# Kernel tuning notes

Measured on AMD Instinct MI355X. Metric: run time of the kernel, lower is better.

Reference implementation:

```python
import jax, jax.numpy as jnp
import numpy as np

N = 20000        # atoms in batch
E = 640000       # edges (avg degree 32)
NG = 1000        # molecules (graphs)
H = 128          # hidden_channels = num_filters
G = 50           # num_gaussians
L = 6            # num_interactions
CUTOFF = 10.0
LOG2 = float(np.log(2.0))


def ssp(x):
    # ShiftedSoftplus: softplus(x) - log(2)
    return jax.nn.softplus(x) - jnp.asarray(LOG2, x.dtype)


def setup_inputs() -> dict:
    key = jax.random.key(0)
    ks = jax.random.split(key, 16)
    pos = jax.random.normal(ks[0], (N, 3), dtype=jnp.float32) * 3.0
    z = jax.random.randint(ks[1], (N,), 1, 100)  # avoid padding_idx 0
    batch = jnp.sort(jax.random.randint(ks[2], (N,), 0, NG))
    edge_index = jax.random.randint(ks[3], (2, E), 0, N)
    # avoid self-loops (zero distance -> nan grad of norm)
    row, col = edge_index[0], edge_index[1]
    col = jnp.where(col == row, (col + 1) % N, col)
    edge_index = jnp.stack([row, col])

    def lin(k, fi, fo, stacked=False):
        shape = (L, fi, fo) if stacked else (fi, fo)
        return (jax.random.normal(k, shape, dtype=jnp.float32) / np.sqrt(fi)).astype(jnp.float32)

    emb = jax.random.normal(ks[4], (100, H), dtype=jnp.float32)
    emb = emb.at[0].set(0.0)  # padding_idx=0
    inp = {
        "pos": pos, "z": z, "batch": batch, "edge_index": edge_index,
        "emb": emb,
        "mlp_w1": lin(ks[5], G, H, True), "mlp_b1": jnp.zeros((L, H), jnp.float32),
        "mlp_w2": lin(ks[6], H, H, True), "mlp_b2": jnp.zeros((L, H), jnp.float32),
        "aw_w": lin(ks[7], H, H, True), "aw_b": jnp.zeros((L, H), jnp.float32),
        "out_w1": lin(ks[8], H, H, True), "out_b1": jnp.zeros((L, H), jnp.float32),
        "out_w2": lin(ks[9], H, H, True), "out_b2": jnp.zeros((L, H), jnp.float32),
        "head_w1": lin(ks[10], H, H // 2), "head_b1": jnp.zeros((H // 2,), jnp.float32),
        "head_w2": lin(ks[11], H // 2, 1), "head_b2": jnp.zeros((1,), jnp.float32),
    }
    return inp


def reference(pos, z, batch, edge_index, emb,
              mlp_w1, mlp_b1, mlp_w2, mlp_b2,
              aw_w, aw_b, out_w1, out_b1, out_w2, out_b2,
              head_w1, head_b1, head_w2, head_b2):
    row, col = edge_index[0], edge_index[1]
    # edge distances
    diff = pos[row] - pos[col]                       # [E,3]
    d = jnp.sqrt(jnp.sum(diff * diff, axis=-1))      # [E]
    # Gaussian smearing
    offset = jnp.linspace(0.0, CUTOFF, G)
    coeff = -0.5 / (offset[1] - offset[0]) ** 2
    ea = jnp.exp(coeff * (d[:, None] - offset[None, :]) ** 2)  # [E,G]
    # cosine cutoff
    C = 0.5 * (jnp.cos(d * jnp.pi / CUTOFF) + 1.0)             # [E]

    h = emb[z]                                                 # [N,H]
    for l in range(L):
        hw = h @ aw_w[l] + aw_b[l]                             # atom-wise linear
        W = ssp(ssp(ea @ mlp_w1[l] + mlp_b1[l]) @ mlp_w2[l] + mlp_b2[l]) * C[:, None]  # [E,H]
        msg = hw[row] * W                                      # gather + filter
        conv = jax.ops.segment_sum(msg, col, num_segments=N)   # scatter-add to targets
        upd = ssp(conv @ out_w1[l] + out_b1[l]) @ out_w2[l] + out_b2[l]
        h = h + upd                                            # residual
    y = ssp(h @ head_w1 + head_b1) @ head_w2 + head_b2         # [N,1]
    return jax.ops.segment_sum(y, batch, num_segments=NG)      # [NG,1]
```

## Files before the change

### kernel.cpp

```cpp
#include <hip/hip_runtime.h>
#include <math.h>

#define HID 128
#define NG_GAUSS 50
#define TBL_P 8192
#define TBL_DMAX 12.8f
#define TBL_DT (TBL_DMAX / (float)TBL_P)
#define TBL_INV_DT ((float)TBL_P / TBL_DMAX)
#define PI_F 3.14159265358979323846f
#define NB 8

typedef short bf16x8 __attribute__((ext_vector_type(8)));
typedef float f32x4 __attribute__((ext_vector_type(4)));

__device__ __forceinline__ float ssp_f(float x) {
  float e = __expf(-fabsf(x));
  return fmaxf(x, 0.f) + __logf(1.f + e) - 0.69314718055994530942f;
}
__device__ __forceinline__ unsigned short f2bf(float x) {
  unsigned u = __float_as_uint(x);
  unsigned r = (u + 0x7FFFu + ((u >> 16) & 1u)) >> 16;
  return (unsigned short)r;
}

__global__ __launch_bounds__(256) void k_edge_pre(
    const float* __restrict__ pos, const int* __restrict__ ei,
    int E, int* __restrict__ epack, int* __restrict__ deg)
{
  int e = blockIdx.x * 256 + threadIdx.x;
  if (e >= E) return;
  int r = ei[e];
  int c = ei[E + e];
  float dx = pos[3*r+0] - pos[3*c+0];
  float dy = pos[3*r+1] - pos[3*c+1];
  float dz = pos[3*r+2] - pos[3*c+2];
  float d = sqrtf(dx*dx + dy*dy + dz*dz);
  int i0 = (int)(d * TBL_INV_DT + 0.5f);
  if (i0 >= TBL_P) { epack[e] = -1; return; }
  epack[e] = (r << 13) | i0;
  atomicAdd(&deg[c * NB + (r >> 12)], 1);
}

__global__ __launch_bounds__(1024) void k_scan1(
    const int* __restrict__ deg, int* __restrict__ ptr,
    int* __restrict__ bsum, int M)
{
  __shared__ int wsum[16];
  int base = blockIdx.x * 2048;
  int t = threadIdx.x;
  int i0 = base + 2 * t;
  int v0 = (i0 < M) ? deg[i0] : 0;
  int v1 = (i0 + 1 < M) ? deg[i0 + 1] : 0;
  int s = v0 + v1;
  int lane = t & 63, w = t >> 6;
  int ps = s;
  for (int o = 1; o < 64; o <<= 1) { int x = __shfl_up(ps, o); if (lane >= o) ps += x; }
  if (lane == 63) wsum[w] = ps;
  __syncthreads();
  if (w == 0 && lane < 16) {
    int v = wsum[lane];
    int pv = v;
    for (int o = 1; o < 16; o <<= 1) { int x = __shfl_up(pv, o); if (lane >= o) pv += x; }
    wsum[lane] = pv - v;
  }
  __syncthreads();
  int ex = wsum[w] + ps - s;
  if (i0 < M) ptr[i0] = ex;
  if (i0 + 1 < M) ptr[i0 + 1] = ex + v0;
  if (t == 1023) bsum[blockIdx.x] = ex + s;
}

__global__ __launch_bounds__(1024) void k_scan2(int* __restrict__ bsum, int G)
{
  __shared__ int wsum[16];
  int t = threadIdx.x;
  int s = (t < G) ? bsum[t] : 0;
  int lane = t & 63, w = t >> 6;
  int ps = s;
  for (int o = 1; o < 64; o <<= 1) { int x = __shfl_up(ps, o); if (lane >= o) ps += x; }
  if (lane == 63) wsum[w] = ps;
  __syncthreads();
  if (w == 0 && lane < 16) {
    int v = wsum[lane];
    int pv = v;
    for (int o = 1; o < 16; o <<= 1) { int x = __shfl_up(pv, o); if (lane >= o) pv += x; }
    wsum[lane] = pv - v;
  }
  __syncthreads();
  int ex = wsum[w] + ps - s;
  if (t < G) bsum[t] = ex;
  if (t == G - 1) bsum[G] = ex + s;
}

__global__ __launch_bounds__(1024) void k_scan3(
    int* __restrict__ ptr, const int* __restrict__ bsum, int M, int G)
{
  int base = blockIdx.x * 2048;
  int t = threadIdx.x;
  int add = bsum[blockIdx.x];
  int i0 = base + 2 * t;
  if (i0 < M) ptr[i0] += add;
  if (i0 + 1 < M) ptr[i0 + 1] += add;
  if (blockIdx.x == 0 && t == 0) ptr[M] = bsum[G];
}

__global__ __launch_bounds__(256) void k_csr_scatter(
    const int* __restrict__ col, const int* __restrict__ epack,
    const int* __restrict__ ptr, int* __restrict__ cursor,
    int* __restrict__ csr, int E)
{
  int e = blockIdx.x * 256 + threadIdx.x;
  if (e >= E) return;
  int p = epack[e];
  if (p < 0) return;
  int c = col[e];
  int idx = c * NB + ((p >> 13) >> 12);
  int slot = ptr[idx] + atomicAdd(&cursor[idx], 1);
  csr[slot] = p;
}

__global__ __launch_bounds__(256) void k_wprep(
    const float* __restrict__ aw_w, const float* __restrict__ out_w1,
    const float* __restrict__ out_w2, const float* __restrict__ mlp_w2,
    const float* __restrict__ mlp_w1, const float* __restrict__ head_w1,
    unsigned short* __restrict__ awt, unsigned short* __restrict__ o1t,
    unsigned short* __restrict__ o2t, unsigned short* __restrict__ m2t,
    unsigned short* __restrict__ m1t, unsigned short* __restrict__ hwt)
{
  __shared__ float Wl[64][132];
  int l = blockIdx.x, t = blockIdx.y;
  int k0 = blockIdx.z * 64;
  const float* src; unsigned short* dst; int K; int NCOL = 128;
  switch (t) {
    case 0:  src = aw_w;   dst = awt; K = 128; break;
    case 1:  src = out_w1; dst = o1t; K = 128; break;
    case 2:  src = out_w2; dst = o2t; K = 128; break;
    case 3:  src = mlp_w2; dst = m2t; K = 128; break;
    case 4:  src = mlp_w1; dst = m1t; K = NG_GAUSS; break;
    default:
      if (l) return;
      src = head_w1; dst = hwt; K = 128; NCOL = 64; break;
  }
  src += (long)l * K * NCOL;
  dst += (long)l * 128 * 128;
  const int tid = threadIdx.x;
  for (int idx = tid; idx < 64 * 128; idx += 256) {
    int kk = idx >> 7, n = idx & 127;
    int k = k0 + kk;
    Wl[kk][n] = (k < K && n < NCOL) ? src[(long)k * NCOL + n] : 0.f;
  }
  __syncthreads();
  for (int idx = tid; idx < 128 * 8; idx += 256) {
    int n = idx >> 3, pl = idx & 7;
    int p = (k0 >> 3) + pl;
    int q = p ^ (n & 7);
    int kk = (q << 3) - k0;
    ushort4 lo = make_ushort4(f2bf(Wl[kk+0][n]), f2bf(Wl[kk+1][n]),
                              f2bf(Wl[kk+2][n]), f2bf(Wl[kk+3][n]));
    ushort4 hi = make_ushort4(f2bf(Wl[kk+4][n]), f2bf(Wl[kk+5][n]),
                              f2bf(Wl[kk+6][n]), f2bf(Wl[kk+7][n]));
    *(ushort4*)(dst + ((long)n << 7) + (p << 3)) = lo;
    *(ushort4*)(dst + ((long)n << 7) + (p << 3) + 4) = hi;
  }
}

__global__ void k_ea_build(unsigned short* __restrict__ EA)
{
  int p = blockIdx.x;
  int g = threadIdx.x;
  float v = 0.f;
  if (g < NG_GAUSS) {
    float step = 10.0f / 49.0f;
    float off = g * step;
    float coeff = -0.5f / (step * step);
    float t = p * TBL_DT - off;
    v = __expf(coeff * t * t);
  }
  EA[p * 128 + g] = f2bf(v);
}

__global__ __launch_bounds__(256) void k_h_init(
    const float4* __restrict__ emb4, const int* __restrict__ z,
    float4* __restrict__ h4, ushort4* __restrict__ hb4, int N)
{
  int idx = blockIdx.x * 256 + threadIdx.x;
  if (idx >= N * 32) return;
  int n = idx >> 5, c = idx & 31;
  float4 v = emb4[z[n] * 32 + c];
  h4[idx] = v;
  hb4[idx] = make_ushort4(f2bf(v.x), f2bf(v.y), f2bf(v.z), f2bf(v.w));
}

__global__ __launch_bounds__(256) void k_fused(
    const unsigned short* __restrict__ X, long xstr,
    const unsigned short* __restrict__ Wa, long wastr,
    const float* __restrict__ ba, long bastr,
    const unsigned short* __restrict__ Wb, long wbstr,
    const float* __restrict__ bb, long bbstr,
    const float* __restrict__ R,
    void* __restrict__ out1, long o1str, int o1_bf16, int actB, int mulC,
    float dscale,
    const unsigned short* __restrict__ Wc, const float* __restrict__ bc,
    unsigned short* __restrict__ out2,
    const float* __restrict__ hw2, const float* __restrict__ hb2,
    const int* __restrict__ batchp, float* __restrict__ outp,
    int M)
{
  __shared__ unsigned short Xs[32][128];
  __shared__ unsigned short Wbuf[128][128];

  const int l = blockIdx.y;
  const int m0 = blockIdx.x * 32;
  const int tid = threadIdx.x;
  const unsigned short* Xb = X + (long)l * xstr;

  for (int idx = tid; idx < 512; idx += 256) {
    int r = idx >> 4, c = idx & 15;
    int m = m0 + r;
    int4 v = make_int4(0, 0, 0, 0);
    if (m < M) v = *(const int4*)(Xb + (long)m * 128 + c * 8);
    *(int4*)&Xs[r][(c ^ (r & 7)) << 3] = v;
  }
  {
    const unsigned short* W0 = Wa ? (Wa + (long)l * wastr) : (Wb + (long)l * wbstr);
    const int4* s = (const int4*)W0;
    int4* d = (int4*)Wbuf;
    for (int i = tid; i < 2048; i += 256) d[i] = s[i];
  }
  __syncthreads();

  const int wv = tid >> 6, lane = tid & 63;
  const int wr = wv >> 1, wc = wv & 1;
  const int lr = lane & 15, lk = lane >> 4;
  const int arow = (wr << 4) | lr;

  f32x4 acc[4];
  auto zacc = [&]() {
#pragma unroll
    for (int i = 0; i < 4; ++i)
#pragma unroll
      for (int j = 0; j < 4; ++j) acc[i][j] = 0.f;
  };
  auto gemm = [&]() {
#pragma unroll
    for (int kc = 0; kc < 4; ++kc) {
      int q = (kc << 2) | lk;
      bf16x8 a = *(const bf16x8*)&Xs[arow][(q ^ (arow & 7)) << 3];
#pragma unroll
      for (int nt = 0; nt < 4; ++nt) {
        int n = (wc << 6) | (nt << 4) | lr;
        bf16x8 b = *(const bf16x8*)(&Wbuf[0][0] + n * 128 + ((q ^ (n & 7)) << 3));
        acc[nt] = __builtin_amdgcn_mfma_f32_16x16x32_bf16(a, b, acc[nt], 0, 0, 0);
      }
    }
  };

  if (Wa) {
    const float* bab = ba + (long)l * bastr;
    zacc();
    gemm();
    __syncthreads();
#pragma unroll
    for (int nt = 0; nt < 4; ++nt) {
      int col = (wc << 6) | (nt << 4) | lr;
      float bv = bab[col];
#pragma unroll
      for (int r2 = 0; r2 < 4; ++r2) {
        int row = (wr << 4) | (lk << 2) | r2;
        float v2 = ssp_f(acc[nt][r2] + bv);
        int cch = col >> 3;
        Xs[row][((cch ^ (row & 7)) << 3) | (col & 7)] = f2bf(v2);
      }
    }
    {
      const int4* s = (const int4*)(Wb + (long)l * wbstr);
      int4* d = (int4*)Wbuf;
      for (int i = tid; i < 2048; i += 256) d[i] = s[i];
    }
    __syncthreads();
  }

  const float* bbb = bb + (long)l * bbstr;
  zacc();
  gemm();
  __syncthreads();

#pragma unroll
  for (int nt = 0; nt < 4; ++nt) {
    int col = (wc << 6) | (nt << 4) | lr;
    float bv = bbb[col];
#pragma unroll
    for (int r2 = 0; r2 < 4; ++r2) {
      int row = (wr << 4) | (lk << 2) | r2;
      int m = m0 + row;
      float v2 = acc[nt][r2] + bv;
      if (actB) v2 = ssp_f(v2);
      if (R && m < M) v2 += R[(long)m * 128 + col];
      if (mulC) {
        float d = (float)m * dscale;
        v2 *= 0.5f * (__cosf(d * (PI_F / 10.0f)) + 1.0f);
      }
      if (m < M && out1) {
        if (o1_bf16)
          ((unsigned short*)out1)[(long)l * o1str + (long)m * 128 + col] = f2bf(v2);
        else
          ((float*)out1)[(long)l * o1str + (long)m * 128 + col] = v2;
      }
      if (Wc) {
        int cch = col >> 3;
        Xs[row][((cch ^ (row & 7)) << 3) | (col & 7)] = f2bf(v2);
      }
    }
  }

  if (Wc) {
    {
      const int4* s = (const int4*)Wc;
      int4* d = (int4*)Wbuf;
      for (int i = tid; i < 2048; i += 256) d[i] = s[i];
    }
    __syncthreads();
    zacc();
    gemm();
    if (hw2) {
      if (wc == 0) {
        float b1v[4], w2v[4];
#pragma unroll
        for (int nt = 0; nt < 4; ++nt) {
          int col = (nt << 4) | lr;
          b1v[nt] = bc[col];
          w2v[nt] = hw2[col];
        }
        float bias2 = hb2[0];
#pragma unroll
        for (int r2 = 0; r2 < 4; ++r2) {
          float sv = 0.f;
#pragma unroll
          for (int nt = 0; nt < 4; ++nt)
            sv += ssp_f(acc[nt][r2] + b1v[nt]) * w2v[nt];
          sv += __shfl_xor(sv, 1);
          sv += __shfl_xor(sv, 2);
          sv += __shfl_xor(sv, 4);
          sv += __shfl_xor(sv, 8);
          if (lr == 0) {
            int m = m0 + (wr << 4) + (lk << 2) + r2;
            if (m < M) atomicAdd(&outp[batchp[m]], sv + bias2);
          }
        }
      }
    } else {
#pragma unroll
      for (int nt = 0; nt < 4; ++nt) {
        int col = (wc << 6) | (nt << 4) | lr;
        float bv = bc[col];
#pragma unroll
        for (int r2 = 0; r2 < 4; ++r2) {
          int row = (wr << 4) | (lk << 2) | r2;
          int m = m0 + row;
          if (m < M)
            out2[(long)m * 128 + col] = f2bf(acc[nt][r2] + bv);
        }
      }
    }
  }
}

__global__ __launch_bounds__(256) void k_conv(
    const int* __restrict__ csr, const int* __restrict__ ptr,
    const unsigned short* __restrict__ T, const unsigned short* __restrict__ hw,
    unsigned short* __restrict__ convb, int N)
{
  int wid = __builtin_amdgcn_readfirstlane((blockIdx.x * 256 + threadIdx.x) >> 6);
  int lane = threadIdx.x & 63;
  if (wid >= N) return;
  int s = __builtin_amdgcn_readfirstlane(ptr[wid * NB]);
  int e = __builtin_amdgcn_readfirstlane(ptr[wid * NB + NB]);
  const int la = lane << 1;
  float ax[8], ay[8];
#pragma unroll
  for (int i = 0; i < 8; ++i) { ax[i] = 0.f; ay[i] = 0.f; }
  int j = s;
  if (j + 8 <= e) {
    int cc[8];
#pragma unroll
    for (int i = 0; i < 8; ++i) cc[i] = __builtin_amdgcn_readfirstlane(csr[j + i]);
    for (; j + 16 <= e; j += 8) {
      unsigned tv[8], hv[8];
#pragma unroll
      for (int i = 0; i < 8; ++i) {
        unsigned pr = (unsigned)cc[i];
        tv[i] = *(const unsigned*)(T + ((size_t)(pr & 8191u) << 7) + la);
        hv[i] = *(const unsigned*)(hw + ((size_t)(pr >> 13) << 7) + la);
      }
#pragma unroll
      for (int i = 0; i < 8; ++i) cc[i] = __builtin_amdgcn_readfirstlane(csr[j + 8 + i]);
#pragma unroll
      for (int i = 0; i < 8; ++i) {
        float w0 = __uint_as_float(tv[i] << 16), w1 = __uint_as_float(tv[i] & 0xffff0000u);
        float h0 = __uint_as_float(hv[i] << 16), h1 = __uint_as_float(hv[i] & 0xffff0000u);
        ax[i] = fmaf(w0, h0, ax[i]); ay[i] = fmaf(w1, h1, ay[i]);
      }
    }
    {
      unsigned tv[8], hv[8];
#pragma unroll
      for (int i = 0; i < 8; ++i) {
        unsigned pr = (unsigned)cc[i];
        tv[i] = *(const unsigned*)(T + ((size_t)(pr & 8191u) << 7) + la);
        hv[i] = *(const unsigned*)(hw + ((size_t)(pr >> 13) << 7) + la);
      }
#pragma unroll
      for (int i = 0; i < 8; ++i) {
        float w0 = __uint_as_float(tv[i] << 16), w1 = __uint_as_float(tv[i] & 0xffff0000u);
        float h0 = __uint_as_float(hv[i] << 16), h1 = __uint_as_float(hv[i] & 0xffff0000u);
        ax[i] = fmaf(w0, h0, ax[i]); ay[i] = fmaf(w1, h1, ay[i]);
      }
    }
    j += 8;
  }
  for (; j < e; ++j) {
    unsigned pr = (unsigned)__builtin_amdgcn_readfirstlane(csr[j]);
    unsigned tv = *(const unsigned*)(T + ((size_t)(pr & 8191u) << 7) + la);
    unsigned hv = *(const unsigned*)(hw + ((size_t)(pr >> 13) << 7) + la);
    float w0 = __uint_as_float(tv << 16), w1 = __uint_as_float(tv & 0xffff0000u);
    float h0 = __uint_as_float(hv << 16), h1 = __uint_as_float(hv & 0xffff0000u);
    ax[0] = fmaf(w0, h0, ax[0]); ay[0] = fmaf(w1, h1, ay[0]);
  }
  float axs = ((ax[0] + ax[1]) + (ax[2] + ax[3])) + ((ax[4] + ax[5]) + (ax[6] + ax[7]));
  float ays = ((ay[0] + ay[1]) + (ay[2] + ay[3])) + ((ay[4] + ay[5]) + (ay[6] + ay[7]));
  unsigned outw = (unsigned)f2bf(axs) | ((unsigned)f2bf(ays) << 16);
  *(unsigned*)(convb + ((size_t)wid << 7) + la) = outw;
}

extern "C" void kernel_launch(void* const* d_in, const int* in_sizes, int n_in,
                              void* d_out, int out_size, void* d_ws, size_t ws_size,
                              hipStream_t stream) {
  (void)n_in; (void)ws_size;
  const float* pos     = (const float*)d_in[0];
  const int*   z       = (const int*)d_in[1];
  const int*   batch   = (const int*)d_in[2];
  const int*   ei      = (const int*)d_in[3];
  const float* emb     = (const float*)d_in[4];
  const float* mlp_w1  = (const float*)d_in[5];
  const float* mlp_b1  = (const float*)d_in[6];
  const float* mlp_w2  = (const float*)d_in[7];
  const float* mlp_b2  = (const float*)d_in[8];
  const float* aw_w    = (const float*)d_in[9];
  const float* aw_b    = (const float*)d_in[10];
  const float* out_w1  = (const float*)d_in[11];
  const float* out_b1  = (const float*)d_in[12];
  const float* out_w2  = (const float*)d_in[13];
  const float* out_b2  = (const float*)d_in[14];
  const float* head_w1 = (const float*)d_in[15];
  const float* head_b1 = (const float*)d_in[16];
  const float* head_w2 = (const float*)d_in[17];
  const float* head_b2 = (const float*)d_in[18];

  const int N  = in_sizes[0] / 3;
  const int E  = in_sizes[3] / 2;
  const int NG = out_size;
  const int L  = in_sizes[5] / (NG_GAUSS * HID);

  char* ws = (char*)d_ws;
  size_t off = 0;
  auto alloc = [&](size_t bytes) -> void* {
    off = (off + 255) & ~(size_t)255;
    void* p = ws + off;
    off += bytes;
    return p;
  };

  const size_t nh = (size_t)N * HID;
  float* h_buf = (float*)alloc(nh * 4 > (size_t)E * 4 ? nh * 4 : (size_t)E * 4);
  int*   epack = (int*)h_buf;
  unsigned short* hb    = (unsigned short*)alloc(nh * 2);
  unsigned short* hw    = (unsigned short*)alloc(nh * 2);
  unsigned short* convb = (unsigned short*)alloc(
      nh * 2 > (size_t)TBL_P * 128 * 2 ? nh * 2 : (size_t)TBL_P * 128 * 2);
  unsigned short* EA    = convb;
  int* csr = (int*)alloc((size_t)E * 4);
  unsigned short* T   = (unsigned short*)alloc((size_t)L * TBL_P * 128 * 2);
  unsigned short* awt = (unsigned short*)alloc((size_t)L * 16384 * 2);
  unsigned short* o1t = (unsigned short*)alloc((size_t)L * 16384 * 2);
  unsigned short* o2t = (unsigned short*)alloc((size_t)L * 16384 * 2);
  unsigned short* m2t = (unsigned short*)alloc((size_t)L * 16384 * 2);
  unsigned short* m1t = (unsigned short*)alloc((size_t)L * 16384 * 2);
  unsigned short* hwt = (unsigned short*)alloc((size_t)16384 * 2);
  int* deg    = (int*)alloc((size_t)N * NB * 4);
  int* ptr    = (int*)alloc(((size_t)N * NB + 1) * 4);
  int* cursor = (int*)alloc((size_t)N * NB * 4);
  int* bsum   = (int*)alloc((size_t)1024 * 4);

  const int M = N * NB;
  const int G = (M + 2047) / 2048;

  hipMemsetAsync(deg, 0, (size_t)M * 4, stream);
  hipMemsetAsync(cursor, 0, (size_t)M * 4, stream);
  hipMemsetAsync(d_out, 0, (size_t)NG * 4, stream);

  int egrid = (E + 255) / 256;
  k_edge_pre<<<egrid, 256, 0, stream>>>(pos, ei, E, epack, deg);
  k_scan1<<<G, 1024, 0, stream>>>(deg, ptr, bsum, M);
  k_scan2<<<1, 1024, 0, stream>>>(bsum, G);
  k_scan3<<<G, 1024, 0, stream>>>(ptr, bsum, M, G);
  k_csr_scatter<<<egrid, 256, 0, stream>>>(ei + E, epack, ptr, cursor, csr, E);

  k_wprep<<<dim3(L, 6, 2), 256, 0, stream>>>(aw_w, out_w1, out_w2, mlp_w2,
                                             mlp_w1, head_w1,
                                             awt, o1t, o2t, m2t, m1t, hwt);
  k_ea_build<<<TBL_P, 128, 0, stream>>>(EA);

  k_fused<<<dim3(TBL_P / 32, L), 256, 0, stream>>>(
      EA, 0L,
      m1t, 16384L, mlp_b1, 128L,
      m2t, 16384L, mlp_b2, 128L,
      (const float*)0,
      T, (long)TBL_P * 128, 1 , 1 , 1 , TBL_DT,
      (const unsigned short*)0, (const float*)0, (unsigned short*)0,
      (const float*)0, (const float*)0, (const int*)0, (float*)0,
      TBL_P);

  k_h_init<<<(N * 32 + 255) / 256, 256, 0, stream>>>(
      (const float4*)emb, z, (float4*)h_buf, (ushort4*)hb, N);

  const int ngrid = (N + 31) / 32;
  const int wgrid = (N * 64 + 255) / 256;

  k_fused<<<dim3(ngrid, 1), 256, 0, stream>>>(
      hb, 0L,
      (const unsigned short*)0, 0L, (const float*)0, 0L,
      awt, 0L, aw_b, 0L,
      (const float*)0,
      hw, 0L, 1 , 0, 0, 0.f,
      (const unsigned short*)0, (const float*)0, (unsigned short*)0,
      (const float*)0, (const float*)0, (const int*)0, (float*)0,
      N);

  for (int l = 0; l < L; ++l) {
    k_conv<<<wgrid, 256, 0, stream>>>(
        csr, ptr, T + (size_t)l * TBL_P * 128, hw, convb, N);
    const int last = (l + 1 == L);
    const unsigned short* Wc = last ? hwt : (awt + (size_t)(l + 1) * 16384);
    const float* bc = last ? head_b1 : (aw_b + (size_t)(l + 1) * 128);
    k_fused<<<dim3(ngrid, 1), 256, 0, stream>>>(
        convb, 0L,
        o1t + (size_t)l * 16384, 0L, out_b1 + (size_t)l * 128, 0L,
        o2t + (size_t)l * 16384, 0L, out_b2 + (size_t)l * 128, 0L,
        h_buf,
        last ? (void*)0 : (void*)h_buf, 0L, 0 , 0 , 0, 0.f,
        Wc, bc, last ? (unsigned short*)0 : hw,
        last ? head_w2 : (const float*)0, last ? head_b2 : (const float*)0,
        last ? batch : (const int*)0, last ? (float*)d_out : (float*)0,
        N);
  }
}
```

Before: 389.5 us.

## Store residual state in bf16, halve filter table, and refine CSR source buckets

The residual hidden state h is now kept only in bf16 and updated in place in the fused update kernel. This replaces the fp32 h buffer plus its separate bf16 copy and cuts residual read/write traffic. The distance lookup table shrinks from 8192 to 4096 points, so the per-layer filter table gathered in the conv kernel is smaller and more cache-resident, at the cost of coarser distance resolution. The CSR source bucketing doubles from 8 to 16 buckets per target to improve gather locality on hw. Accumulating the residual in bf16 across six layers risks a loss of accuracy.

```diff
diff --git a/kernel.cpp b/kernel.cpp
--- a/kernel.cpp
+++ b/kernel.cpp
@@ -3,12 +3,13 @@
 
 #define HID 128
 #define NG_GAUSS 50
-#define TBL_P 8192
+#define TBL_P 4096
 #define TBL_DMAX 12.8f
 #define TBL_DT (TBL_DMAX / (float)TBL_P)
 #define TBL_INV_DT ((float)TBL_P / TBL_DMAX)
 #define PI_F 3.14159265358979323846f
-#define NB 8
+#define NB 16
+#define BSH 11
 
 typedef short bf16x8 __attribute__((ext_vector_type(8)));
 typedef float f32x4 __attribute__((ext_vector_type(4)));
@@ -21,6 +22,9 @@
   unsigned u = __float_as_uint(x);
   unsigned r = (u + 0x7FFFu + ((u >> 16) & 1u)) >> 16;
   return (unsigned short)r;
+}
+__device__ __forceinline__ float bf2f_s(unsigned short v) {
+  return __uint_as_float((unsigned)v << 16);
 }
 
 __global__ __launch_bounds__(256) void k_edge_pre(
@@ -38,7 +42,7 @@
   int i0 = (int)(d * TBL_INV_DT + 0.5f);
   if (i0 >= TBL_P) { epack[e] = -1; return; }
   epack[e] = (r << 13) | i0;
-  atomicAdd(&deg[c * NB + (r >> 12)], 1);
+  atomicAdd(&deg[c * NB + (r >> BSH)], 1);
 }
 
 __global__ __launch_bounds__(1024) void k_scan1(
@@ -114,7 +118,7 @@
   int p = epack[e];
   if (p < 0) return;
   int c = col[e];
-  int idx = c * NB + ((p >> 13) >> 12);
+  int idx = c * NB + ((p >> 13) >> BSH);
   int slot = ptr[idx] + atomicAdd(&cursor[idx], 1);
   csr[slot] = p;
 }
@@ -180,15 +184,19 @@
 }
 
 __global__ __launch_bounds__(256) void k_h_init(
-    const float4* __restrict__ emb4, const int* __restrict__ z,
-    float4* __restrict__ h4, ushort4* __restrict__ hb4, int N)
+    const float* __restrict__ emb, const int* __restrict__ z,
+    unsigned short* __restrict__ h, int N)
 {
   int idx = blockIdx.x * 256 + threadIdx.x;
-  if (idx >= N * 32) return;
-  int n = idx >> 5, c = idx & 31;
-  float4 v = emb4[z[n] * 32 + c];
-  h4[idx] = v;
-  hb4[idx] = make_ushort4(f2bf(v.x), f2bf(v.y), f2bf(v.z), f2bf(v.w));
+  if (idx >= N * 16) return;
+  int n = idx >> 4, c = idx & 15;
+  const float* er = emb + (long)z[n] * 128 + (c << 3);
+  float4 lo = *(const float4*)er;
+  float4 hi = *(const float4*)(er + 4);
+  alignas(16) unsigned short u[8];
+  u[0]=f2bf(lo.x); u[1]=f2bf(lo.y); u[2]=f2bf(lo.z); u[3]=f2bf(lo.w);
+  u[4]=f2bf(hi.x); u[5]=f2bf(hi.y); u[6]=f2bf(hi.z); u[7]=f2bf(hi.w);
+  *(int4*)(h + (long)n * 128 + (c << 3)) = *(int4*)u;
 }
 
 __global__ __launch_bounds__(256) void k_fused(
@@ -197,7 +205,8 @@
     const float* __restrict__ ba, long bastr,
     const unsigned short* __restrict__ Wb, long wbstr,
     const float* __restrict__ bb, long bbstr,
-    const float* __restrict__ R,
+    unsigned short* __restrict__ R,
+    int r_write,
     void* __restrict__ out1, long o1str, int o1_bf16, int actB, int mulC,
     float dscale,
     const unsigned short* __restrict__ Wc, const float* __restrict__ bc,
@@ -295,7 +304,10 @@
       int m = m0 + row;
       float v2 = acc[nt][r2] + bv;
       if (actB) v2 = ssp_f(v2);
-      if (R && m < M) v2 += R[(long)m * 128 + col];
+      if (R && m < M) {
+        v2 += bf2f_s(R[(long)m * 128 + col]);
+        if (r_write) R[(long)m * 128 + col] = f2bf(v2);
+      }
       if (mulC) {
         float d = (float)m * dscale;
         v2 *= 0.5f * (__cosf(d * (PI_F / 10.0f)) + 1.0f);
@@ -389,7 +401,7 @@
 #pragma unroll
       for (int i = 0; i < 8; ++i) {
         unsigned pr = (unsigned)cc[i];
-        tv[i] = *(const unsigned*)(T + ((size_t)(pr & 8191u) << 7) + la);
+        tv[i] = *(const unsigned*)(T + ((size_t)(pr & 4095u) << 7) + la);
         hv[i] = *(const unsigned*)(hw + ((size_t)(pr >> 13) << 7) + la);
       }
 #pragma unroll
@@ -406,7 +418,7 @@
 #pragma unroll
       for (int i = 0; i < 8; ++i) {
         unsigned pr = (unsigned)cc[i];
-        tv[i] = *(const unsigned*)(T + ((size_t)(pr & 8191u) << 7) + la);
+        tv[i] = *(const unsigned*)(T + ((size_t)(pr & 4095u) << 7) + la);
         hv[i] = *(const unsigned*)(hw + ((size_t)(pr >> 13) << 7) + la);
       }
 #pragma unroll
@@ -420,7 +432,7 @@
   }
   for (; j < e; ++j) {
     unsigned pr = (unsigned)__builtin_amdgcn_readfirstlane(csr[j]);
-    unsigned tv = *(const unsigned*)(T + ((size_t)(pr & 8191u) << 7) + la);
+    unsigned tv = *(const unsigned*)(T + ((size_t)(pr & 4095u) << 7) + la);
     unsigned hv = *(const unsigned*)(hw + ((size_t)(pr >> 13) << 7) + la);
     float w0 = __uint_as_float(tv << 16), w1 = __uint_as_float(tv & 0xffff0000u);
     float h0 = __uint_as_float(hv << 16), h1 = __uint_as_float(hv & 0xffff0000u);
@@ -470,13 +482,12 @@
     return p;
   };
 
-  const size_t nh = (size_t)N * HID;
-  float* h_buf = (float*)alloc(nh * 4 > (size_t)E * 4 ? nh * 4 : (size_t)E * 4);
-  int*   epack = (int*)h_buf;
-  unsigned short* hb    = (unsigned short*)alloc(nh * 2);
-  unsigned short* hw    = (unsigned short*)alloc(nh * 2);
+  const size_t nh2 = (size_t)N * HID * 2;
+  unsigned short* h = (unsigned short*)alloc(nh2 > (size_t)E * 4 ? nh2 : (size_t)E * 4);
+  int* epack = (int*)h;
+  unsigned short* hw    = (unsigned short*)alloc(nh2);
   unsigned short* convb = (unsigned short*)alloc(
-      nh * 2 > (size_t)TBL_P * 128 * 2 ? nh * 2 : (size_t)TBL_P * 128 * 2);
+      nh2 > (size_t)TBL_P * 128 * 2 ? nh2 : (size_t)TBL_P * 128 * 2);
   unsigned short* EA    = convb;
   int* csr = (int*)alloc((size_t)E * 4);
   unsigned short* T   = (unsigned short*)alloc((size_t)L * TBL_P * 128 * 2);
@@ -489,7 +500,7 @@
   int* deg    = (int*)alloc((size_t)N * NB * 4);
   int* ptr    = (int*)alloc(((size_t)N * NB + 1) * 4);
   int* cursor = (int*)alloc((size_t)N * NB * 4);
-  int* bsum   = (int*)alloc((size_t)1024 * 4);
+  int* bsum   = (int*)alloc((size_t)4096 * 4);
 
   const int M = N * NB;
   const int G = (M + 2047) / 2048;
@@ -514,23 +525,22 @@
       EA, 0L,
       m1t, 16384L, mlp_b1, 128L,
       m2t, 16384L, mlp_b2, 128L,
-      (const float*)0,
+      (unsigned short*)0, 0,
       T, (long)TBL_P * 128, 1 , 1 , 1 , TBL_DT,
       (const unsigned short*)0, (const float*)0, (unsigned short*)0,
       (const float*)0, (const float*)0, (const int*)0, (float*)0,
       TBL_P);
 
-  k_h_init<<<(N * 32 + 255) / 256, 256, 0, stream>>>(
-      (const float4*)emb, z, (float4*)h_buf, (ushort4*)hb, N);
+  k_h_init<<<(N * 16 + 255) / 256, 256, 0, stream>>>(emb, z, h, N);
 
   const int ngrid = (N + 31) / 32;
   const int wgrid = (N * 64 + 255) / 256;
 
   k_fused<<<dim3(ngrid, 1), 256, 0, stream>>>(
-      hb, 0L,
+      h, 0L,
       (const unsigned short*)0, 0L, (const float*)0, 0L,
       awt, 0L, aw_b, 0L,
-      (const float*)0,
+      (unsigned short*)0, 0,
       hw, 0L, 1 , 0, 0, 0.f,
       (const unsigned short*)0, (const float*)0, (unsigned short*)0,
       (const float*)0, (const float*)0, (const int*)0, (float*)0,
@@ -546,8 +556,8 @@
         convb, 0L,
         o1t + (size_t)l * 16384, 0L, out_b1 + (size_t)l * 128, 0L,
         o2t + (size_t)l * 16384, 0L, out_b2 + (size_t)l * 128, 0L,
-        h_buf,
-        last ? (void*)0 : (void*)h_buf, 0L, 0 , 0 , 0, 0.f,
+        h, last ? 0 : 1 ,
+        (void*)0, 0L, 0, 0 , 0, 0.f,
         Wc, bc, last ? (unsigned short*)0 : hw,
         last ? head_w2 : (const float*)0, last ? head_b2 : (const float*)0,
         last ? batch : (const int*)0, last ? (float*)d_out : (float*)0,
```

Result: faster. 360.7 us (-7.4%).
